# Performance work log

Measured on AMD Instinct MI355X. Metric: run time of the kernel, lower is better.

## Reference

```python
import jax, jax.numpy as jnp
import numpy as np

NEG_SLOPE = 0.2


def gat_conv(x, edge_index, W, a_src, a_dst, b, concat):
    """PyG-style GATConv: add self-loops, linear, edge attention, scatter-softmax, scatter-add."""
    N = x.shape[0]
    H, C = a_src.shape
    loop = jnp.arange(N)
    src = jnp.concatenate([edge_index[0], loop])  # source j (messages flow j -> i)
    dst = jnp.concatenate([edge_index[1], loop])  # target i (aggregation node)
    h = (x @ W).reshape(N, H, C)                  # [N,H,C]
    alpha_s = jnp.sum(h * a_src, axis=-1)         # [N,H]
    alpha_d = jnp.sum(h * a_dst, axis=-1)         # [N,H]
    e = jax.nn.leaky_relu(alpha_s[src] + alpha_d[dst], NEG_SLOPE)  # [E,H]
    # numerically stable scatter-softmax over edges grouped by destination node
    m = jax.ops.segment_max(e, dst, num_segments=N)                # [N,H]
    ex = jnp.exp(e - m[dst])
    denom = jax.ops.segment_sum(ex, dst, num_segments=N)           # [N,H]
    alpha = ex / (denom[dst] + 1e-16)                              # [E,H]
    out = jax.ops.segment_sum(h[src] * alpha[:, :, None], dst, num_segments=N)  # [N,H,C]
    out = out.reshape(N, H * C) if concat else out.mean(axis=1)
    return out + b


def setup_inputs() -> dict:
    key = jax.random.key(0)
    ks = jax.random.split(key, 12)
    N, E, F_IN, HID, OUT, HEADS = 100000, 1600000, 128, 128, 64, 4
    C1 = HID // HEADS
    x = jax.random.normal(ks[0], (N, F_IN), dtype=jnp.float32)
    edge_index = jax.random.randint(ks[1], (2, E), 0, N, dtype=jnp.int64)
    s = 0.05
    return {
        "x": x,
        "edge_index": edge_index,
        "W1": jax.random.normal(ks[2], (F_IN, HEADS * C1), dtype=jnp.float32) * s,
        "a_src1": jax.random.normal(ks[3], (HEADS, C1), dtype=jnp.float32) * s,
        "a_dst1": jax.random.normal(ks[4], (HEADS, C1), dtype=jnp.float32) * s,
        "b1": jnp.zeros((HEADS * C1,), dtype=jnp.float32),
        "W2": jax.random.normal(ks[5], (HID, OUT), dtype=jnp.float32) * s,
        "a_src2": jax.random.normal(ks[6], (1, OUT), dtype=jnp.float32) * s,
        "a_dst2": jax.random.normal(ks[7], (1, OUT), dtype=jnp.float32) * s,
        "b2": jnp.zeros((OUT,), dtype=jnp.float32),
    }


def reference(x, edge_index, W1, a_src1, a_dst1, b1, W2, a_src2, a_dst2, b2):
    h = jax.nn.elu(gat_conv(x, edge_index, W1, a_src1, a_dst1, b1, concat=True))
    # F.dropout(p=0.5, training=False) is the identity in eval mode
    out = gat_conv(h, edge_index, W2, a_src2, a_dst2, b2, concat=False)
    return out
```

## Files before the change

### kernel.cpp

```cpp
#include <hip/hip_runtime.h>
#include <hip/hip_fp16.h>
#include <math.h>


#define BSH 9
#define DPB 512
#define NBK 256
#define CH1 16384

__device__ __forceinline__ float exp2_fast(float x) {
#if __has_builtin(__builtin_amdgcn_exp2f)
    return __builtin_amdgcn_exp2f(x);
#else
    return exp2f(x);
#endif
}


__global__ void zero_small(unsigned* p) {
    p[threadIdx.x] = 0;
}

__global__ __launch_bounds__(256) void bucket_hist(const int* __restrict__ ei, int E, int N,
                                                   unsigned* __restrict__ bcount) {
    __shared__ unsigned hist[NBK];
    int t = threadIdx.x;
    hist[t] = 0;
    __syncthreads();
    int Etot = E + N;
    for (int k = blockIdx.x * 256 + t; k < Etot; k += gridDim.x * 256) {
        int d = (k < E) ? ei[E + k] : (k - E);
        atomicAdd(&hist[d >> BSH], 1u);
    }
    __syncthreads();
    unsigned c = hist[t];
    if (c) atomicAdd(&bcount[t], c);
}

__global__ void scan_buckets(const unsigned* __restrict__ bcount, unsigned* __restrict__ bbase,
                             unsigned* __restrict__ bcursor) {
    __shared__ unsigned s[NBK];
    int t = threadIdx.x;
    unsigned v = bcount[t];
    s[t] = v;
    __syncthreads();
    for (int o = 1; o < NBK; o <<= 1) {
        unsigned add = (t >= o) ? s[t - o] : 0;
        __syncthreads();
        s[t] += add;
        __syncthreads();
    }
    unsigned excl = s[t] - v;
    bbase[t] = excl;
    bcursor[t] = excl;
    if (t == NBK - 1) bbase[NBK] = excl + v;
}

__global__ __launch_bounds__(256) void bucket_scatter(const int* __restrict__ ei, int E, int N,
                                                      unsigned* __restrict__ bcursor,
                                                      uint2* __restrict__ rec) {
    __shared__ unsigned hist[NBK];
    __shared__ unsigned base[NBK];
    int t = threadIdx.x;
    hist[t] = 0;
    __syncthreads();
    int Etot = E + N;
    int k0 = blockIdx.x * CH1;
    int k1 = min(k0 + CH1, Etot);
    for (int k = k0 + t; k < k1; k += 256) {
        int d = (k < E) ? ei[E + k] : (k - E);
        atomicAdd(&hist[d >> BSH], 1u);
    }
    __syncthreads();
    unsigned c = hist[t];
    base[t] = c ? atomicAdd(&bcursor[t], c) : 0u;
    hist[t] = 0;
    __syncthreads();
    for (int k = k0 + t; k < k1; k += 256) {
        int s, d;
        if (k < E) { s = ei[k]; d = ei[E + k]; } else { s = d = k - E; }
        int b = d >> BSH;
        unsigned r = atomicAdd(&hist[b], 1u);
        rec[base[b] + r] = make_uint2((unsigned)s, (unsigned)d);
    }
}

__global__ __launch_bounds__(256) void bucket_sort(const uint2* __restrict__ rec,
                                                   const unsigned* __restrict__ bbase,
                                                   int* __restrict__ offs, int* __restrict__ srcs,
                                                   int N, int Etot) {
    __shared__ unsigned hist[DPB];
    __shared__ unsigned tsum[256];
    int t = threadIdx.x, bb = blockIdx.x;
    unsigned r0 = bbase[bb], r1 = bbase[bb + 1];
    hist[t] = 0;
    hist[t + 256] = 0;
    __syncthreads();
    int dlo = bb << BSH;
    for (unsigned k = r0 + t; k < r1; k += 256) {
        uint2 e = rec[k];
        atomicAdd(&hist[e.y - dlo], 1u);
    }
    __syncthreads();
    unsigned h0 = hist[2 * t], h1 = hist[2 * t + 1];
    tsum[t] = h0 + h1;
    __syncthreads();
    for (int o = 1; o < 256; o <<= 1) {
        unsigned a = (t >= o) ? tsum[t - o] : 0;
        __syncthreads();
        tsum[t] += a;
        __syncthreads();
    }
    unsigned tb = tsum[t] - (h0 + h1);
    int d0 = dlo + 2 * t;
    if (d0 < N) offs[d0] = (int)(r0 + tb);
    if (d0 + 1 < N) offs[d0 + 1] = (int)(r0 + tb + h0);
    hist[2 * t] = tb;
    hist[2 * t + 1] = tb + h0;
    __syncthreads();
    for (unsigned k = r0 + t; k < r1; k += 256) {
        uint2 e = rec[k];
        unsigned r = atomicAdd(&hist[e.y - dlo], 1u);
        srcs[r0 + r] = (int)e.x;
    }
    if (bb == 0 && t == 0) offs[N] = Etot;
}


template <int NC, typename InT, typename OutT>
__global__ __launch_bounds__(256) void gemm_k128(const InT* __restrict__ A,
                                                 const float* __restrict__ B,
                                                 OutT* __restrict__ C, int M) {
    constexpr int BM = 64, BK = 32, K = 128;
    constexpr int TPR = NC / 4;
    constexpr int R = BM / (256 / TPR);
    __shared__ float AsT[BK][BM + 4];
    __shared__ float Bs[BK][NC];
    int tid = threadIdx.x;
    int tx = tid % TPR, ty = tid / TPR;
    int rowBase = blockIdx.x * BM;
    float acc[R][4] = {};
    for (int k0 = 0; k0 < K; k0 += BK) {
#pragma unroll
        for (int i = 0; i < 4; ++i) {
            int lin = tid + i * 256;
            int row = lin >> 4;
            int kp = lin & 15;
            int grow = rowBase + row;
            if (grow >= M) grow = M - 1;
            float2 v;
            if constexpr (sizeof(InT) == 2) {
                __half2 hv = *reinterpret_cast<const __half2*>((const __half*)A + (size_t)grow * K + k0 + kp * 2);
                v = __half22float2(hv);
            } else {
                v = *reinterpret_cast<const float2*>((const float*)A + (size_t)grow * K + k0 + kp * 2);
            }
            AsT[kp * 2][row] = v.x;
            AsT[kp * 2 + 1][row] = v.y;
        }
#pragma unroll
        for (int i = 0; i < (BK * NC) / 1024; ++i) {
            int lin = tid + i * 256;
            int row = lin / (NC / 4);
            int col4 = lin % (NC / 4);
            float4 v = *reinterpret_cast<const float4*>(B + (size_t)(k0 + row) * NC + col4 * 4);
            *reinterpret_cast<float4*>(&Bs[row][col4 * 4]) = v;
        }
        __syncthreads();
#pragma unroll
        for (int kk = 0; kk < BK; ++kk) {
            float4 bv = *reinterpret_cast<const float4*>(&Bs[kk][tx * 4]);
            float a[R];
#pragma unroll
            for (int r4 = 0; r4 < R; r4 += 4) {
                float4 av = *reinterpret_cast<const float4*>(&AsT[kk][ty * R + r4]);
                a[r4] = av.x; a[r4 + 1] = av.y; a[r4 + 2] = av.z; a[r4 + 3] = av.w;
            }
#pragma unroll
            for (int r = 0; r < R; ++r) {
                acc[r][0] = fmaf(a[r], bv.x, acc[r][0]);
                acc[r][1] = fmaf(a[r], bv.y, acc[r][1]);
                acc[r][2] = fmaf(a[r], bv.z, acc[r][2]);
                acc[r][3] = fmaf(a[r], bv.w, acc[r][3]);
            }
        }
        __syncthreads();
    }
#pragma unroll
    for (int r = 0; r < R; ++r) {
        int grow = rowBase + ty * R + r;
        if (grow < M) {
            if constexpr (sizeof(OutT) == 2) {
                __half2 p0 = __floats2half2_rn(acc[r][0], acc[r][1]);
                __half2 p1 = __floats2half2_rn(acc[r][2], acc[r][3]);
                __half2* cp = reinterpret_cast<__half2*>((__half*)C + (size_t)grow * NC + tx * 4);
                cp[0] = p0;
                cp[1] = p1;
            } else {
                float4 v = make_float4(acc[r][0], acc[r][1], acc[r][2], acc[r][3]);
                *reinterpret_cast<float4*>((float*)C + (size_t)grow * NC + tx * 4) = v;
            }
        }
    }
}


#define LOG2E 1.44269504088896f

__global__ __launch_bounds__(256) void alphas1_kernel(const __half* __restrict__ h,
                                                      const float* __restrict__ a_src,
                                                      const float* __restrict__ a_dst,
                                                      float* __restrict__ as,
                                                      float* __restrict__ ad, int N) {
    int wid = (blockIdx.x * blockDim.x + threadIdx.x) >> 6;
    int lane = threadIdx.x & 63;
    if (wid >= N) return;
    const __half2* hp = reinterpret_cast<const __half2*>(h);
    float2 hv = __half22float2(hp[(size_t)wid * 64 + lane]);
    float s = hv.x * a_src[2 * lane] + hv.y * a_src[2 * lane + 1];
    float d = hv.x * a_dst[2 * lane] + hv.y * a_dst[2 * lane + 1];
#pragma unroll
    for (int o = 1; o < 16; o <<= 1) {
        s += __shfl_xor(s, o, 64);
        d += __shfl_xor(d, o, 64);
    }
    if ((lane & 15) == 0) {
        int head = lane >> 4;
        as[(size_t)wid * 4 + head] = s * LOG2E;
        ad[(size_t)wid * 4 + head] = d * LOG2E;
    }
}

__global__ __launch_bounds__(256) void alphas2_kernel(const __half* __restrict__ h,
                                                      const float* __restrict__ a_src,
                                                      const float* __restrict__ a_dst,
                                                      float* __restrict__ as,
                                                      float* __restrict__ ad, int N) {
    int wid = (blockIdx.x * blockDim.x + threadIdx.x) >> 6;
    int lane = threadIdx.x & 63;
    if (wid >= N) return;
    float hv = __half2float(h[(size_t)wid * 64 + lane]);
    float s = hv * a_src[lane];
    float d = hv * a_dst[lane];
#pragma unroll
    for (int o = 1; o < 64; o <<= 1) {
        s += __shfl_xor(s, o, 64);
        d += __shfl_xor(d, o, 64);
    }
    if (lane == 0) {
        as[wid] = s * LOG2E;
        ad[wid] = d * LOG2E;
    }
}


__global__ __launch_bounds__(256) void aggregate1(const __half* __restrict__ h,
                                                  const float* __restrict__ as,
                                                  const float* __restrict__ ad,
                                                  const int* __restrict__ offs,
                                                  const int* __restrict__ srcs,
                                                  const float* __restrict__ bias,
                                                  __half* __restrict__ out, int N) {
    int wid = (blockIdx.x * blockDim.x + threadIdx.x) >> 6;
    int lane = threadIdx.x & 63;
    if (wid >= N) return;
    int head = lane >> 4;
    float adv = ad[(size_t)wid * 4 + head];
    int e0 = offs[wid], e1 = offs[wid + 1];
    const __half2* hp = reinterpret_cast<const __half2*>(h);
    float acc0 = 0.f, acc1 = 0.f, den = 0.f;
    int e = e0;
    for (; e + 8 <= e1; e += 8) {
        int j[8]; float t[8]; __half2 hh[8];
#pragma unroll
        for (int u = 0; u < 8; ++u) j[u] = srcs[e + u];
#pragma unroll
        for (int u = 0; u < 8; ++u) t[u] = as[(size_t)j[u] * 4 + head] + adv;
#pragma unroll
        for (int u = 0; u < 8; ++u) hh[u] = hp[(size_t)j[u] * 64 + lane];
#pragma unroll
        for (int u = 0; u < 8; ++u) {
            float x = exp2_fast(fmaxf(t[u], 0.2f * t[u]));
            float2 hv = __half22float2(hh[u]);
            acc0 = fmaf(x, hv.x, acc0);
            acc1 = fmaf(x, hv.y, acc1);
            den += x;
        }
    }
    for (; e < e1; ++e) {
        int j = srcs[e];
        float t = as[(size_t)j * 4 + head] + adv;
        float x = exp2_fast(fmaxf(t, 0.2f * t));
        float2 hv = __half22float2(hp[(size_t)j * 64 + lane]);
        acc0 = fmaf(x, hv.x, acc0);
        acc1 = fmaf(x, hv.y, acc1);
        den += x;
    }
    float r = 1.0f / (den + 1e-16f);
    float v0 = acc0 * r + bias[2 * lane];
    float v1 = acc1 * r + bias[2 * lane + 1];
    v0 = (v0 > 0.f) ? v0 : expm1f(v0);
    v1 = (v1 > 0.f) ? v1 : expm1f(v1);
    reinterpret_cast<__half2*>(out)[(size_t)wid * 64 + lane] = __floats2half2_rn(v0, v1);
}

__global__ __launch_bounds__(256) void aggregate2(const __half* __restrict__ h,
                                                  const float* __restrict__ as,
                                                  const float* __restrict__ ad,
                                                  const int* __restrict__ offs,
                                                  const int* __restrict__ srcs,
                                                  const float* __restrict__ bias,
                                                  float* __restrict__ out, int N) {
    int wid = (blockIdx.x * blockDim.x + threadIdx.x) >> 6;
    int lane = threadIdx.x & 63;
    if (wid >= N) return;
    float adv = ad[wid];
    int e0 = offs[wid], e1 = offs[wid + 1];
    float acc = 0.f, den = 0.f;
    int e = e0;
    for (; e + 8 <= e1; e += 8) {
        int j[8]; float t[8]; __half hh[8];
#pragma unroll
        for (int u = 0; u < 8; ++u) j[u] = srcs[e + u];
#pragma unroll
        for (int u = 0; u < 8; ++u) t[u] = as[j[u]] + adv;
#pragma unroll
        for (int u = 0; u < 8; ++u) hh[u] = h[(size_t)j[u] * 64 + lane];
#pragma unroll
        for (int u = 0; u < 8; ++u) {
            float x = exp2_fast(fmaxf(t[u], 0.2f * t[u]));
            acc = fmaf(x, __half2float(hh[u]), acc);
            den += x;
        }
    }
    for (; e < e1; ++e) {
        int j = srcs[e];
        float t = as[j] + adv;
        float x = exp2_fast(fmaxf(t, 0.2f * t));
        acc = fmaf(x, __half2float(h[(size_t)j * 64 + lane]), acc);
        den += x;
    }
    float r = 1.0f / (den + 1e-16f);
    out[(size_t)wid * 64 + lane] = acc * r + bias[lane];
}


extern "C" void kernel_launch(void* const* d_in, const int* in_sizes, int n_in,
                              void* d_out, int out_size, void* d_ws, size_t ws_size,
                              hipStream_t stream) {
    const float* x      = (const float*)d_in[0];
    const int*   ei     = (const int*)d_in[1];
    const float* W1     = (const float*)d_in[2];
    const float* a_src1 = (const float*)d_in[3];
    const float* a_dst1 = (const float*)d_in[4];
    const float* b1     = (const float*)d_in[5];
    const float* W2     = (const float*)d_in[6];
    const float* a_src2 = (const float*)d_in[7];
    const float* a_dst2 = (const float*)d_in[8];
    const float* b2     = (const float*)d_in[9];
    float* out = (float*)d_out;

    const int N = out_size / 64;
    const int E = in_sizes[1] / 2;
    const int Etot = E + N;

    size_t off = 0;
    auto carve = [&](size_t bytes) -> void* {
        void* p = (char*)d_ws + off;
        off += (bytes + 255) & ~(size_t)255;
        return p;
    };
    __half* h1      = (__half*)carve((size_t)N * 128 * 2);
    __half* hmid    = (__half*)carve((size_t)N * 128 * 2);
    float* as1      = (float*)carve((size_t)N * 4 * 4);
    float* ad1      = (float*)carve((size_t)N * 4 * 4);
    float* as2      = (float*)carve((size_t)N * 4);
    float* ad2      = (float*)carve((size_t)N * 4);
    int*   offs     = (int*)carve((size_t)(N + 1) * 4);
    int*   srcs     = (int*)carve((size_t)Etot * 4);
    uint2* rec      = (uint2*)carve((size_t)Etot * 8);
    unsigned* bcount  = (unsigned*)carve(NBK * 4);
    unsigned* bbase   = (unsigned*)carve((NBK + 1) * 4);
    unsigned* bcursor = (unsigned*)carve(NBK * 4);
    __half* h2      = h1;

    zero_small<<<1, 256, 0, stream>>>(bcount);
    bucket_hist<<<128, 256, 0, stream>>>(ei, E, N, bcount);
    scan_buckets<<<1, 256, 0, stream>>>(bcount, bbase, bcursor);
    bucket_scatter<<<(Etot + CH1 - 1) / CH1, 256, 0, stream>>>(ei, E, N, bcursor, rec);
    bucket_sort<<<(N + DPB - 1) / DPB, 256, 0, stream>>>(rec, bbase, offs, srcs, N, Etot);

    gemm_k128<128, float, __half><<<(N + 63) / 64, 256, 0, stream>>>(x, W1, h1, N);
    alphas1_kernel<<<(N + 3) / 4, 256, 0, stream>>>(h1, a_src1, a_dst1, as1, ad1, N);
    aggregate1<<<(N + 3) / 4, 256, 0, stream>>>(h1, as1, ad1, offs, srcs, b1, hmid, N);

    gemm_k128<64, __half, __half><<<(N + 63) / 64, 256, 0, stream>>>(hmid, W2, h2, N);
    alphas2_kernel<<<(N + 3) / 4, 256, 0, stream>>>(h2, a_src2, a_dst2, as2, ad2, N);
    aggregate2<<<(N + 3) / 4, 256, 0, stream>>>(h2, as2, ad2, offs, srcs, b2, out, N);
}
```

Baseline: 436.2 us.

## Fuse attention-logit computation into GEMM epilogue and restructure aggregation loops

Removes the separate alphas1/alphas2 kernels by computing the per-head source and destination attention dot products in the GEMM epilogue, using warp shuffles across the column threads of each head. This saves two launches and a reread of h. The aggregation loops are rewritten into a single 4-wide loop with clamped indices and masked weights in place of the 8-wide loop plus scalar tail, and they use 32-bit unsigned index math. zero_small is replaced by hipMemsetAsync. One side effect is that the logits are now computed from fp32 accumulators instead of rounded fp16 values.

```diff
diff --git a/kernel.cpp b/kernel.cpp
--- a/kernel.cpp
+++ b/kernel.cpp
@@ -7,6 +7,7 @@
 #define DPB 512
 #define NBK 256
 #define CH1 16384
+#define LOG2E 1.44269504088896f
 
 __device__ __forceinline__ float exp2_fast(float x) {
 #if __has_builtin(__builtin_amdgcn_exp2f)
@@ -16,10 +17,6 @@
 #endif
 }
 
-
-__global__ void zero_small(unsigned* p) {
-    p[threadIdx.x] = 0;
-}
 
 __global__ __launch_bounds__(256) void bucket_hist(const int* __restrict__ ei, int E, int N,
                                                    unsigned* __restrict__ bcount) {
@@ -127,13 +124,18 @@
 }
 
 
-template <int NC, typename InT, typename OutT>
+template <int NC, int H, typename InT, typename OutT>
 __global__ __launch_bounds__(256) void gemm_k128(const InT* __restrict__ A,
                                                  const float* __restrict__ B,
-                                                 OutT* __restrict__ C, int M) {
+                                                 OutT* __restrict__ C,
+                                                 const float* __restrict__ a_src,
+                                                 const float* __restrict__ a_dst,
+                                                 float* __restrict__ as,
+                                                 float* __restrict__ ad, int M) {
     constexpr int BM = 64, BK = 32, K = 128;
     constexpr int TPR = NC / 4;
     constexpr int R = BM / (256 / TPR);
+    constexpr int TXH = TPR / H;
     __shared__ float AsT[BK][BM + 4];
     __shared__ float Bs[BK][NC];
     int tid = threadIdx.x;
@@ -186,10 +188,13 @@
         }
         __syncthreads();
     }
+    float4 asv = *reinterpret_cast<const float4*>(a_src + tx * 4);
+    float4 adv = *reinterpret_cast<const float4*>(a_dst + tx * 4);
 #pragma unroll
     for (int r = 0; r < R; ++r) {
         int grow = rowBase + ty * R + r;
-        if (grow < M) {
+        bool live = grow < M;
+        if (live) {
             if constexpr (sizeof(OutT) == 2) {
                 __half2 p0 = __floats2half2_rn(acc[r][0], acc[r][1]);
                 __half2 p1 = __floats2half2_rn(acc[r][2], acc[r][3]);
@@ -201,55 +206,18 @@
                 *reinterpret_cast<float4*>((float*)C + (size_t)grow * NC + tx * 4) = v;
             }
         }
-    }
-}
-
-
-#define LOG2E 1.44269504088896f
-
-__global__ __launch_bounds__(256) void alphas1_kernel(const __half* __restrict__ h,
-                                                      const float* __restrict__ a_src,
-                                                      const float* __restrict__ a_dst,
-                                                      float* __restrict__ as,
-                                                      float* __restrict__ ad, int N) {
-    int wid = (blockIdx.x * blockDim.x + threadIdx.x) >> 6;
-    int lane = threadIdx.x & 63;
-    if (wid >= N) return;
-    const __half2* hp = reinterpret_cast<const __half2*>(h);
-    float2 hv = __half22float2(hp[(size_t)wid * 64 + lane]);
-    float s = hv.x * a_src[2 * lane] + hv.y * a_src[2 * lane + 1];
-    float d = hv.x * a_dst[2 * lane] + hv.y * a_dst[2 * lane + 1];
-#pragma unroll
-    for (int o = 1; o < 16; o <<= 1) {
-        s += __shfl_xor(s, o, 64);
-        d += __shfl_xor(d, o, 64);
-    }
-    if ((lane & 15) == 0) {
-        int head = lane >> 4;
-        as[(size_t)wid * 4 + head] = s * LOG2E;
-        ad[(size_t)wid * 4 + head] = d * LOG2E;
-    }
-}
-
-__global__ __launch_bounds__(256) void alphas2_kernel(const __half* __restrict__ h,
-                                                      const float* __restrict__ a_src,
-                                                      const float* __restrict__ a_dst,
-                                                      float* __restrict__ as,
-                                                      float* __restrict__ ad, int N) {
-    int wid = (blockIdx.x * blockDim.x + threadIdx.x) >> 6;
-    int lane = threadIdx.x & 63;
-    if (wid >= N) return;
-    float hv = __half2float(h[(size_t)wid * 64 + lane]);
-    float s = hv * a_src[lane];
-    float d = hv * a_dst[lane];
-#pragma unroll
-    for (int o = 1; o < 64; o <<= 1) {
-        s += __shfl_xor(s, o, 64);
-        d += __shfl_xor(d, o, 64);
-    }
-    if (lane == 0) {
-        as[wid] = s * LOG2E;
-        ad[wid] = d * LOG2E;
+        float ps = acc[r][0] * asv.x + acc[r][1] * asv.y + acc[r][2] * asv.z + acc[r][3] * asv.w;
+        float pd = acc[r][0] * adv.x + acc[r][1] * adv.y + acc[r][2] * adv.z + acc[r][3] * adv.w;
+#pragma unroll
+        for (int o = 1; o < TXH; o <<= 1) {
+            ps += __shfl_xor(ps, o, 64);
+            pd += __shfl_xor(pd, o, 64);
+        }
+        if ((tx & (TXH - 1)) == 0 && live) {
+            int head = tx / TXH;
+            as[(size_t)grow * H + head] = ps * LOG2E;
+            ad[(size_t)grow * H + head] = pd * LOG2E;
+        }
     }
 }
 
@@ -261,47 +229,49 @@
                                                   const int* __restrict__ srcs,
                                                   const float* __restrict__ bias,
                                                   __half* __restrict__ out, int N) {
-    int wid = (blockIdx.x * blockDim.x + threadIdx.x) >> 6;
-    int lane = threadIdx.x & 63;
-    if (wid >= N) return;
-    int head = lane >> 4;
-    float adv = ad[(size_t)wid * 4 + head];
+    unsigned wid = (blockIdx.x * blockDim.x + threadIdx.x) >> 6;
+    unsigned lane = threadIdx.x & 63;
+    if (wid >= (unsigned)N) return;
+    unsigned head = lane >> 4;
+    float adv = ad[wid * 4u + head];
     int e0 = offs[wid], e1 = offs[wid + 1];
+    int e1m1 = e1 - 1;
     const __half2* hp = reinterpret_cast<const __half2*>(h);
     float acc0 = 0.f, acc1 = 0.f, den = 0.f;
-    int e = e0;
-    for (; e + 8 <= e1; e += 8) {
-        int j[8]; float t[8]; __half2 hh[8];
-#pragma unroll
-        for (int u = 0; u < 8; ++u) j[u] = srcs[e + u];
-#pragma unroll
-        for (int u = 0; u < 8; ++u) t[u] = as[(size_t)j[u] * 4 + head] + adv;
-#pragma unroll
-        for (int u = 0; u < 8; ++u) hh[u] = hp[(size_t)j[u] * 64 + lane];
-#pragma unroll
-        for (int u = 0; u < 8; ++u) {
-            float x = exp2_fast(fmaxf(t[u], 0.2f * t[u]));
-            float2 hv = __half22float2(hh[u]);
-            acc0 = fmaf(x, hv.x, acc0);
-            acc1 = fmaf(x, hv.y, acc1);
-            den += x;
-        }
-    }
-    for (; e < e1; ++e) {
-        int j = srcs[e];
-        float t = as[(size_t)j * 4 + head] + adv;
-        float x = exp2_fast(fmaxf(t, 0.2f * t));
-        float2 hv = __half22float2(hp[(size_t)j * 64 + lane]);
-        acc0 = fmaf(x, hv.x, acc0);
-        acc1 = fmaf(x, hv.y, acc1);
-        den += x;
+    for (int e = e0; e < e1; e += 4) {
+        unsigned j0 = (unsigned)srcs[min(e, e1m1)];
+        unsigned j1 = (unsigned)srcs[min(e + 1, e1m1)];
+        unsigned j2 = (unsigned)srcs[min(e + 2, e1m1)];
+        unsigned j3 = (unsigned)srcs[min(e + 3, e1m1)];
+        float t0 = as[j0 * 4u + head] + adv;
+        float t1 = as[j1 * 4u + head] + adv;
+        float t2 = as[j2 * 4u + head] + adv;
+        float t3 = as[j3 * 4u + head] + adv;
+        __half2 h0 = hp[j0 * 64u + lane];
+        __half2 h1 = hp[j1 * 64u + lane];
+        __half2 h2 = hp[j2 * 64u + lane];
+        __half2 h3 = hp[j3 * 64u + lane];
+        float x0 = exp2_fast(fmaxf(t0, 0.2f * t0));
+        float x1 = exp2_fast(fmaxf(t1, 0.2f * t1));
+        float x2 = exp2_fast(fmaxf(t2, 0.2f * t2));
+        float x3 = exp2_fast(fmaxf(t3, 0.2f * t3));
+        x1 = (e + 1 < e1) ? x1 : 0.f;
+        x2 = (e + 2 < e1) ? x2 : 0.f;
+        x3 = (e + 3 < e1) ? x3 : 0.f;
+        float2 f0 = __half22float2(h0), f1 = __half22float2(h1);
+        float2 f2 = __half22float2(h2), f3 = __half22float2(h3);
+        acc0 = fmaf(x0, f0.x, acc0); acc1 = fmaf(x0, f0.y, acc1);
+        acc0 = fmaf(x1, f1.x, acc0); acc1 = fmaf(x1, f1.y, acc1);
+        acc0 = fmaf(x2, f2.x, acc0); acc1 = fmaf(x2, f2.y, acc1);
+        acc0 = fmaf(x3, f3.x, acc0); acc1 = fmaf(x3, f3.y, acc1);
+        den += (x0 + x1) + (x2 + x3);
     }
     float r = 1.0f / (den + 1e-16f);
     float v0 = acc0 * r + bias[2 * lane];
     float v1 = acc1 * r + bias[2 * lane + 1];
     v0 = (v0 > 0.f) ? v0 : expm1f(v0);
     v1 = (v1 > 0.f) ? v1 : expm1f(v1);
-    reinterpret_cast<__half2*>(out)[(size_t)wid * 64 + lane] = __floats2half2_rn(v0, v1);
+    reinterpret_cast<__half2*>(out)[wid * 64u + lane] = __floats2half2_rn(v0, v1);
 }
 
 __global__ __launch_bounds__(256) void aggregate2(const __half* __restrict__ h,
@@ -311,37 +281,41 @@
                                                   const int* __restrict__ srcs,
                                                   const float* __restrict__ bias,
                                                   float* __restrict__ out, int N) {
-    int wid = (blockIdx.x * blockDim.x + threadIdx.x) >> 6;
-    int lane = threadIdx.x & 63;
-    if (wid >= N) return;
+    unsigned wid = (blockIdx.x * blockDim.x + threadIdx.x) >> 6;
+    unsigned lane = threadIdx.x & 63;
+    if (wid >= (unsigned)N) return;
     float adv = ad[wid];
     int e0 = offs[wid], e1 = offs[wid + 1];
+    int e1m1 = e1 - 1;
     float acc = 0.f, den = 0.f;
-    int e = e0;
-    for (; e + 8 <= e1; e += 8) {
-        int j[8]; float t[8]; __half hh[8];
-#pragma unroll
-        for (int u = 0; u < 8; ++u) j[u] = srcs[e + u];
-#pragma unroll
-        for (int u = 0; u < 8; ++u) t[u] = as[j[u]] + adv;
-#pragma unroll
-        for (int u = 0; u < 8; ++u) hh[u] = h[(size_t)j[u] * 64 + lane];
-#pragma unroll
-        for (int u = 0; u < 8; ++u) {
-            float x = exp2_fast(fmaxf(t[u], 0.2f * t[u]));
-            acc = fmaf(x, __half2float(hh[u]), acc);
-            den += x;
-        }
-    }
-    for (; e < e1; ++e) {
-        int j = srcs[e];
-        float t = as[j] + adv;
-        float x = exp2_fast(fmaxf(t, 0.2f * t));
-        acc = fmaf(x, __half2float(h[(size_t)j * 64 + lane]), acc);
-        den += x;
+    for (int e = e0; e < e1; e += 4) {
+        unsigned j0 = (unsigned)srcs[min(e, e1m1)];
+        unsigned j1 = (unsigned)srcs[min(e + 1, e1m1)];
+        unsigned j2 = (unsigned)srcs[min(e + 2, e1m1)];
+        unsigned j3 = (unsigned)srcs[min(e + 3, e1m1)];
+        float t0 = as[j0] + adv;
+        float t1 = as[j1] + adv;
+        float t2 = as[j2] + adv;
+        float t3 = as[j3] + adv;
+        __half h0 = h[j0 * 64u + lane];
+        __half h1 = h[j1 * 64u + lane];
+        __half h2 = h[j2 * 64u + lane];
+        __half h3 = h[j3 * 64u + lane];
+        float x0 = exp2_fast(fmaxf(t0, 0.2f * t0));
+        float x1 = exp2_fast(fmaxf(t1, 0.2f * t1));
+        float x2 = exp2_fast(fmaxf(t2, 0.2f * t2));
+        float x3 = exp2_fast(fmaxf(t3, 0.2f * t3));
+        x1 = (e + 1 < e1) ? x1 : 0.f;
+        x2 = (e + 2 < e1) ? x2 : 0.f;
+        x3 = (e + 3 < e1) ? x3 : 0.f;
+        acc = fmaf(x0, __half2float(h0), acc);
+        acc = fmaf(x1, __half2float(h1), acc);
+        acc = fmaf(x2, __half2float(h2), acc);
+        acc = fmaf(x3, __half2float(h3), acc);
+        den += (x0 + x1) + (x2 + x3);
     }
     float r = 1.0f / (den + 1e-16f);
-    out[(size_t)wid * 64 + lane] = acc * r + bias[lane];
+    out[wid * 64u + lane] = acc * r + bias[lane];
 }
 
 
@@ -384,17 +358,17 @@
     unsigned* bcursor = (unsigned*)carve(NBK * 4);
     __half* h2      = h1;
 
-    zero_small<<<1, 256, 0, stream>>>(bcount);
+    hipMemsetAsync(bcount, 0, NBK * sizeof(unsigned), stream);
     bucket_hist<<<128, 256, 0, stream>>>(ei, E, N, bcount);
     scan_buckets<<<1, 256, 0, stream>>>(bcount, bbase, bcursor);
     bucket_scatter<<<(Etot + CH1 - 1) / CH1, 256, 0, stream>>>(ei, E, N, bcursor, rec);
     bucket_sort<<<(N + DPB - 1) / DPB, 256, 0, stream>>>(rec, bbase, offs, srcs, N, Etot);
 
-    gemm_k128<128, float, __half><<<(N + 63) / 64, 256, 0, stream>>>(x, W1, h1, N);
-    alphas1_kernel<<<(N + 3) / 4, 256, 0, stream>>>(h1, a_src1, a_dst1, as1, ad1, N);
+    gemm_k128<128, 4, float, __half><<<(N + 63) / 64, 256, 0, stream>>>(
+        x, W1, h1, a_src1, a_dst1, as1, ad1, N);
     aggregate1<<<(N + 3) / 4, 256, 0, stream>>>(h1, as1, ad1, offs, srcs, b1, hmid, N);
 
-    gemm_k128<64, __half, __half><<<(N + 63) / 64, 256, 0, stream>>>(hmid, W2, h2, N);
-    alphas2_kernel<<<(N + 3) / 4, 256, 0, stream>>>(h2, a_src2, a_dst2, as2, ad2, N);
+    gemm_k128<64, 1, __half, __half><<<(N + 63) / 64, 256, 0, stream>>>(
+        hmid, W2, h2, a_src2, a_dst2, as2, ad2, N);
     aggregate2<<<(N + 3) / 4, 256, 0, stream>>>(h2, as2, ad2, offs, srcs, b2, out, N);
 }
```

Result: faster. 407.6 us (-6.6%).
